# Kernel tuning notes

Hardware: AMD Instinct MI355X
Metric: run time of the kernel (lower is better)

Reference implementation:

```python
import jax, jax.numpy as jnp
from jax import lax
import numpy as np

B, T, DIN, DMID, DOUT = 8, 512, 512, 512, 128
KER = (0.15, 0.7, 0.15)  # 3-tap Gaussian blur, midnum fixed at 0.7 (deterministic stand-in for random.uniform(0.55,0.9))


def setup_inputs() -> dict:
    key = jax.random.key(0)
    ks = jax.random.split(key, 14)
    def lin(k, fi, fo):
        s = (6.0 / (fi + fo)) ** 0.5  # xavier-uniform
        return jax.random.uniform(k, (fi, fo), jnp.float32, -s, s)
    def convw(k, co, ci, kh, kw):
        s = (6.0 / (ci * kh * kw + co * kh * kw)) ** 0.5
        return jax.random.uniform(k, (co, ci, kh, kw), jnp.float32, -s, s)
    return {
        "seq": jax.random.normal(ks[0], (B, T, DIN), jnp.float32),
        "len_seq": jax.random.randint(ks[1], (B,), 256, T + 1, jnp.int32),
        "W1": lin(ks[2], DIN, DMID), "b1": jnp.zeros((DMID,), jnp.float32),
        "W2": lin(ks[3], DMID, DMID), "b2": jnp.zeros((DMID,), jnp.float32),
        "W3": lin(ks[4], DMID, DOUT), "b3": jnp.zeros((DOUT,), jnp.float32),
        "c1w": convw(ks[5], 30, 2, 5, 5), "c1b": jnp.zeros((30,), jnp.float32),
        "c2w": convw(ks[6], 30, 30, 5, 5), "c2b": jnp.zeros((30,), jnp.float32),
        "c3w": convw(ks[7], 1, 30, 3, 3), "c3b": jnp.zeros((1,), jnp.float32),
    }


def _mlp(x, W1, b1, W2, b2, W3, b3):
    # SequenceInception: linear-relu-linear-relu-linear, then L2 normalize with nan/inf -> 0
    h = jax.nn.relu(x @ W1 + b1)
    h = jax.nn.relu(h @ W2 + b2)
    o = h @ W3 + b3
    n = jnp.linalg.norm(o, axis=-1, keepdims=True)
    return jnp.nan_to_num(o / n, nan=0.0, posinf=0.0, neginf=0.0)


def _conv(x, w, b, pad):
    y = lax.conv_general_dilated(x, w, (1, 1), ((pad, pad), (pad, pad)),
                                 dimension_numbers=("NCHW", "OIHW", "NCHW"))
    return y + b[None, :, None, None]


def _blur(seq, len_seq):
    # BlurGenerationPair (Tc>4, 3-tap kernel, stride 1 branch), fully batched.
    k0, k1, k2 = KER
    blur = k0 * seq[:, :-2] + k1 * seq[:, 1:-1] + k2 * seq[:, 2:]  # [B, T-2, D]
    blur = jnp.pad(blur, ((0, 0), (0, 2), (0, 0)))
    t = jnp.arange(T)
    out_len = len_seq - 2
    out_mask = (t[None, :] < out_len[:, None]).astype(seq.dtype)      # [B, T]
    avged_seq = blur * out_mask[:, :, None]
    R = jnp.where(t[None] < len_seq[:, None], (t + 1.0) / len_seq[:, None].astype(jnp.float32), 0.0)
    avged_R = jnp.where(t[None] < out_len[:, None], (t + 1.0) / out_len[:, None].astype(jnp.float32), 0.0)
    # SeqtoBlur[b, i+o, i] = ker[o] for column i < out_len[b]
    base = k0 * jnp.eye(T) + k1 * jnp.eye(T, k=-1) + k2 * jnp.eye(T, k=-2)  # [T(row), T(col)]
    SeqtoBlur = base[None, :, :] * out_mask[:, None, :]
    sg = lax.stop_gradient
    return sg(SeqtoBlur), sg(avged_seq), sg(R), sg(avged_R), out_len


def reference(seq, len_seq, W1, b1, W2, b2, W3, b3, c1w, c1b, c2w, c2b, c3w, c3b):
    SeqtoBlur, avged_seq, R, avged_R, avged_len = _blur(seq, len_seq)
    emb_q = _mlp(seq, W1, b1, W2, b2, W3, b3)        # [B, T, DOUT]
    emb_k = _mlp(avged_seq, W1, b1, W2, b2, W3, b3)  # [B, T, DOUT]
    # OPA, batched over B (original asserts batch==1 and loops; same math per sample)
    sq = jnp.sum(emb_q * emb_q, -1)
    sk = jnp.sum(emb_k * emb_k, -1)
    g = jnp.einsum("bqd,bkd->bqk", emb_q, emb_k)
    D = jnp.sqrt(jnp.clip(sq[:, :, None] + sk[:, None, :] - 2.0 * g, 1e-12))  # cdist p=2
    P = jnp.abs(R[:, :, None] - avged_R[:, None, :])                           # 1-D cdist
    A = jnp.stack([D, P], axis=1)                    # [B, 2, T, T]
    A = jax.nn.relu(_conv(A, c1w, c1b, 2))
    A = jax.nn.relu(_conv(A, c2w, c2b, 2))
    A = _conv(A, c3w, c3b, 1)[:, 0] + D              # [B, T, T]
    S = jax.nn.softmax(-A, axis=2)
    At = S / jnp.sum(jnp.abs(S), axis=(1, 2), keepdims=True)  # L1 normalize over T*T
    dis = jnp.sum(D * At, axis=(1, 2))               # [B]
    return S, dis, SeqtoBlur, avged_len
```

## Files before the change

kernel.cpp:

```cpp
#include <hip/hip_runtime.h>
#include <hip/hip_bf16.h>

static constexpr size_t CHW = (size_t)512*512*32;

static constexpr size_t S_OFF    = 0;
static constexpr size_t DIS_OFF  = (size_t)8*512*512;
static constexpr size_t S2B_OFF  = DIS_OFF + 8;
static constexpr size_t ALEN_OFF = S2B_OFF + (size_t)8*512*512;

typedef __attribute__((ext_vector_type(8))) short bf16x8;
typedef __attribute__((ext_vector_type(4))) float f32x4;
typedef __attribute__((ext_vector_type(2))) float f32x2;
typedef __attribute__((ext_vector_type(4))) int   i32x4;

__device__ __forceinline__ unsigned short rne_bf16(float x) {
  unsigned u = __builtin_bit_cast(unsigned, x);
  return (unsigned short)((u + 0x7FFFu + ((u >> 16) & 1u)) >> 16);
}
__device__ __forceinline__ unsigned pack_bf16x2(float lo, float hi) {
  return (unsigned)rne_bf16(lo) | ((unsigned)rne_bf16(hi) << 16);
}
__device__ __forceinline__ float bf2f(short s) {
  return __builtin_bit_cast(float, ((unsigned)(unsigned short)s) << 16);
}
__device__ __forceinline__ int chlog(int p) { return (p & 1) ? 16 + (p >> 1) : (p >> 1); }

__global__ __launch_bounds__(128) void megaprep(
    const float* __restrict__ seq, const int* __restrict__ len,
    const float* __restrict__ W1, const float* __restrict__ W2, const float* __restrict__ W3,
    const float* __restrict__ c1w, const float* __restrict__ c2w, const float* __restrict__ c3w,
    unsigned short* __restrict__ QKb,
    unsigned short* __restrict__ W1T, unsigned short* __restrict__ W2T,
    unsigned short* __restrict__ W3T,
    unsigned short* __restrict__ WB1m, unsigned char* __restrict__ WB2f,
    float* __restrict__ WT3, float* __restrict__ zpage,
    float* __restrict__ R, float* __restrict__ AR, float* __restrict__ alenOut,
    float* __restrict__ s2b) {
  int bid = blockIdx.x, tid = threadIdx.x;
  if (bid < 8192) {
    int t = bid & 511, b = (bid >> 9) & 7, mode = bid >> 12;
    size_t base = ((size_t)b*512 + t)*512 + tid*4;
    float v[4] = {0.f, 0.f, 0.f, 0.f};
    if (mode == 0) {
      float4 a = *(const float4*)&seq[base];
      v[0]=a.x; v[1]=a.y; v[2]=a.z; v[3]=a.w;
    } else {
      int OL = len[b] - 2;
      if (t < OL) {
        float4 a = *(const float4*)&seq[base];
        float4 c = *(const float4*)&seq[base + 512];
        float4 d = *(const float4*)&seq[base + 1024];
        v[0] = 0.15f*a.x + 0.7f*c.x + 0.15f*d.x;
        v[1] = 0.15f*a.y + 0.7f*c.y + 0.15f*d.y;
        v[2] = 0.15f*a.z + 0.7f*c.z + 0.15f*d.z;
        v[3] = 0.15f*a.w + 0.7f*c.w + 0.15f*d.w;
      }
    }
    ushort4 h;
    h.x = rne_bf16(v[0]); h.y = rne_bf16(v[1]);
    h.z = rne_bf16(v[2]); h.w = rne_bf16(v[3]);
    *(ushort4*)&QKb[((size_t)(mode*4096 + b*512 + t))*512 + tid*4] = h;
    return;
  }
  if (bid < 12288) {
    int r = bid - 8192;
    int i = r & 511, b = r >> 9;
    int OL = len[b] - 2;
    int j0 = tid*4;
    float vals[4];
#pragma unroll
    for (int e = 0; e < 4; ++e) {
      int j = j0 + e;
      float x = 0.f;
      if (j < OL) {
        if (j == i)        x = 0.15f;
        else if (j == i-1) x = 0.7f;
        else if (j == i-2) x = 0.15f;
      }
      vals[e] = x;
    }
    *(float4*)&s2b[((size_t)b*512 + i)*512 + j0] =
        make_float4(vals[0],vals[1],vals[2],vals[3]);
    return;
  }
  if (bid < 12320) {
    int r = bid - 12288;
    int b = r >> 2, t = (r & 3)*128 + tid;
    int L = len[b], OL = L - 2;
    R[b*512+t]  = (t < L)  ? (t+1.f)/(float)L  : 0.f;
    AR[b*512+t] = (t < OL) ? (t+1.f)/(float)OL : 0.f;
    if (t == 0) alenOut[b] = (float)OL;
    return;
  }
  if (bid < 13472) {
    int n = bid - 12320;
    const float* W; unsigned short* WT; int col, N;
    if (n < 512)       { W = W1; WT = W1T; col = n;        N = 512; }
    else if (n < 1024) { W = W2; WT = W2T; col = n - 512;  N = 512; }
    else               { W = W3; WT = W3T; col = n - 1024; N = 128; }
    for (int k = tid; k < 512; k += 128)
      WT[(size_t)col*512 + k] = rne_bf16(W[(size_t)k*N + col]);
    return;
  }
  if (tid < 64) zpage[tid] = 0.f;
  for (int i = tid; i < 7168; i += 128) {
    int ts = i >> 8, r = i & 255, oc = r >> 3, ch = r & 7;
    float v = 0.f;
    if (ts < 25 && oc < 30 && ch < 2) v = c1w[oc*50 + ch*25 + ts];
    WB1m[i] = rne_bf16(v);
  }
  for (int i = tid; i < 12800; i += 128) {
    int tap = i >> 9, r = i & 511, oc = r >> 4, jj = r & 15;
    float v0 = (oc < 30 && jj < 30)      ? c2w[(size_t)(oc*30 + jj)*25 + tap]      : 0.f;
    float v1 = (oc < 30 && 16 + jj < 30) ? c2w[(size_t)(oc*30 + 16 + jj)*25 + tap] : 0.f;
    int pk = __builtin_amdgcn_cvt_pk_fp8_f32(v0, v1, 0, false);
    ((unsigned short*)WB2f)[(tap*32 + oc)*16 + jj] = (unsigned short)pk;
  }
  for (int i = tid; i < 288; i += 128) {
    int tap = i >> 5, icp = i & 31;
    int icl = chlog(icp);
    WT3[i] = (icl < 30) ? c3w[icl*9 + tap] : 0.f;
  }
}

template<int OUTMODE>
__global__ __launch_bounds__(256) void gemm_bf(
    const unsigned short* __restrict__ A, const unsigned short* __restrict__ B,
    const float* __restrict__ bias, float* __restrict__ Cf,
    unsigned short* __restrict__ Cb, int M, int N, int K) {
  __shared__ short sA[128*40], sB[64*40];
  int tid = threadIdx.x, l = tid & 63, w = tid >> 6;
  int wm = w >> 1, wn = w & 1;
  int rowBase = blockIdx.y * 128, colBase = blockIdx.x * 64;
  int lr = l & 15, lc = l >> 4;
  f32x4 acc[4][2] = {};
  for (int k0 = 0; k0 < K; k0 += 32) {
    int idx = tid;
#pragma unroll
    for (int it = 0; it < 2; ++it, idx += 256) {
      int row = idx >> 2, c = (idx & 3) * 8;
      *(bf16x8*)&sA[row*40 + c] = *(const bf16x8*)&A[(size_t)(rowBase + row)*K + k0 + c];
    }
    {
      int row = tid >> 2, c = (tid & 3) * 8;
      if (row < 64)
        *(bf16x8*)&sB[row*40 + c] = *(const bf16x8*)&B[(size_t)(colBase + row)*K + k0 + c];
    }
    __syncthreads();
    bf16x8 a[4], b[2];
#pragma unroll
    for (int m = 0; m < 4; ++m)
      a[m] = *(const bf16x8*)&sA[(wm*64 + m*16 + lr)*40 + lc*8];
#pragma unroll
    for (int n = 0; n < 2; ++n)
      b[n] = *(const bf16x8*)&sB[(wn*32 + n*16 + lr)*40 + lc*8];
#pragma unroll
    for (int m = 0; m < 4; ++m)
#pragma unroll
      for (int n = 0; n < 2; ++n)
        acc[m][n] = __builtin_amdgcn_mfma_f32_16x16x32_bf16(a[m], b[n], acc[m][n], 0, 0, 0);
    __syncthreads();
  }
#pragma unroll
  for (int m = 0; m < 4; ++m) {
    int row = rowBase + wm*64 + m*16 + lc*4;
#pragma unroll
    for (int n = 0; n < 2; ++n) {
      int col = colBase + wn*32 + n*16 + lr;
      float bv = bias[col];
#pragma unroll
      for (int j = 0; j < 4; ++j) {
        float v = acc[m][n][j] + bv;
        size_t o = (size_t)(row + j) * N + col;
        if (OUTMODE == 1) Cb[o] = rne_bf16(fmaxf(v, 0.f));
        else              Cf[o] = v;
      }
    }
  }
}

__global__ __launch_bounds__(64) void norm_kernel(const float* __restrict__ EMB,
    unsigned short* __restrict__ Eb, float* __restrict__ sqn) {
  int row = blockIdx.x, tid = threadIdx.x;
  size_t base = (size_t)row * 128;
  float v0 = EMB[base + tid], v1 = EMB[base + tid + 64];
  float ss = v0*v0 + v1*v1;
#pragma unroll
  for (int off = 32; off; off >>= 1) ss += __shfl_xor(ss, off);
  float n = sqrtf(ss);
  float inv = (n > 0.f) ? 1.f/n : 0.f;
  Eb[base + tid]      = rne_bf16(v0 * inv);
  Eb[base + tid + 64] = rne_bf16(v1 * inv);
  if (tid == 0) sqn[row] = ss * inv * inv;
}

__global__ __launch_bounds__(256) void dmat_mfma(const unsigned short* __restrict__ Eb,
    const float* __restrict__ sqn, float* __restrict__ Dm) {
  __shared__ short sQ[64*40], sK[64*40];
  int tid = threadIdx.x, l = tid & 63, w = tid >> 6;
  int wm = w >> 1, wn = w & 1;
  int kBase = blockIdx.x * 64, qBase = blockIdx.y * 64, b = blockIdx.z;
  const unsigned short* Q  = Eb + (size_t)b*512*128;
  const unsigned short* Kp = Eb + (size_t)(4096 + b*512)*128;
  int lr = l & 15, lc = l >> 4;
  f32x4 acc[2][2] = {};
  for (int k0 = 0; k0 < 128; k0 += 32) {
    int row = tid >> 2, c = (tid & 3) * 8;
    *(bf16x8*)&sQ[row*40 + c] = *(const bf16x8*)&Q[(size_t)(qBase + row)*128 + k0 + c];
    *(bf16x8*)&sK[row*40 + c] = *(const bf16x8*)&Kp[(size_t)(kBase + row)*128 + k0 + c];
    __syncthreads();
    bf16x8 q[2], k[2];
#pragma unroll
    for (int m = 0; m < 2; ++m) q[m] = *(const bf16x8*)&sQ[(wm*32 + m*16 + lr)*40 + lc*8];
#pragma unroll
    for (int n = 0; n < 2; ++n) k[n] = *(const bf16x8*)&sK[(wn*32 + n*16 + lr)*40 + lc*8];
#pragma unroll
    for (int m = 0; m < 2; ++m)
#pragma unroll
      for (int n = 0; n < 2; ++n)
        acc[m][n] = __builtin_amdgcn_mfma_f32_16x16x32_bf16(q[m], k[n], acc[m][n], 0, 0, 0);
    __syncthreads();
  }
#pragma unroll
  for (int m = 0; m < 2; ++m) {
#pragma unroll
    for (int n = 0; n < 2; ++n) {
      int k = kBase + wn*32 + n*16 + lr;
      float skv = sqn[4096 + b*512 + k];
#pragma unroll
      for (int j = 0; j < 4; ++j) {
        int q = qBase + wm*32 + m*16 + lc*4 + j;
        float sqv = sqn[b*512 + q];
        float d2 = fmaxf(sqv + skv - 2.f*acc[m][n][j], 1e-12f);
        Dm[((size_t)b*512 + q)*512 + k] = sqrtf(d2);
      }
    }
  }
}

__global__ __launch_bounds__(256) void conv1_mfma(const float* __restrict__ Dm,
    const float* __restrict__ R, const float* __restrict__ AR,
    unsigned char* __restrict__ cbout, const unsigned short* __restrict__ WB1m,
    const float* __restrict__ bias, int b0) {
  __shared__ short tile[36*20*8];
  int tid = threadIdx.x, l = tid & 63, w = tid >> 6;
  int x0 = blockIdx.x * 16, y0 = blockIdx.y * 32, slot = blockIdx.z;
  int b = b0 + slot;
  for (int i = tid; i < 720; i += 256) {
    int r = i / 20, c = i - r*20;
    int gy = y0 - 2 + r, gx = x0 - 2 + c;
    float dv = 0.f, pv = 0.f;
    if ((unsigned)gy < 512u && (unsigned)gx < 512u) {
      dv = Dm[((size_t)b*512 + gy)*512 + gx];
      pv = fabsf(R[b*512 + gy] - AR[b*512 + gx]);
    }
    bf16x8 v = {};
    v[0] = (short)rne_bf16(dv);
    v[1] = (short)rne_bf16(pv);
    *(bf16x8*)&tile[i*8] = v;
  }
  __syncthreads();
  int lr = l & 15, lc = l >> 4;
  f32x4 acc[8][2] = {};
  int wy = w * 8;
  bf16x8 pb0 = *(const bf16x8*)&WB1m[(size_t)lc*256 + lr*8];
  bf16x8 pb1 = *(const bf16x8*)&WB1m[(size_t)lc*256 + (16 + lr)*8];
  __builtin_amdgcn_s_setprio(1);
#pragma unroll
  for (int m = 0; m < 7; ++m) {
    int t = m*4 + lc;
    int ky = t / 5, kx = t - ky*5;
    bool valid = (t < 25);
    bf16x8 b0 = pb0, b1 = pb1;
    if (m < 6) {
      int tn = (m+1)*4 + lc;
      pb0 = *(const bf16x8*)&WB1m[(size_t)tn*256 + lr*8];
      pb1 = *(const bf16x8*)&WB1m[(size_t)tn*256 + (16 + lr)*8];
    }
#pragma unroll
    for (int g = 0; g < 8; ++g) {
      bf16x8 a = {};
      if (valid) a = *(const bf16x8*)&tile[((wy + g + ky)*20 + lr + kx)*8];
      acc[g][0] = __builtin_amdgcn_mfma_f32_16x16x32_bf16(a, b0, acc[g][0], 0, 0, 0);
      acc[g][1] = __builtin_amdgcn_mfma_f32_16x16x32_bf16(a, b1, acc[g][1], 0, 0, 0);
    }
  }
  __builtin_amdgcn_s_setprio(0);
  unsigned char* outp = cbout + (size_t)slot * CHW;
  float bv0 = bias[lr];
  float bv1 = (16 + lr < 30) ? bias[16 + lr] : 0.f;
#pragma unroll
  for (int g = 0; g < 8; ++g) {
    int y = y0 + wy + g;
#pragma unroll
    for (int j = 0; j < 4; ++j) {
      int px = x0 + lc*4 + j;
      size_t ob = ((size_t)y*512 + px)*32;
      int pk = __builtin_amdgcn_cvt_pk_fp8_f32(
          fmaxf(acc[g][0][j] + bv0, 0.f), fmaxf(acc[g][1][j] + bv1, 0.f), 0, false);
      *(unsigned short*)&outp[ob + 2*lr] = (unsigned short)pk;
    }
  }
}

__global__ __launch_bounds__(256, 4) void conv2_mfma(const unsigned char* __restrict__ cbin,
    unsigned char* __restrict__ cbout, const unsigned char* __restrict__ WB2f,
    const float* __restrict__ bias, const float* __restrict__ zpage) {
  __shared__ char tile[36*20*32];
  int tid = threadIdx.x, l = tid & 63, w = tid >> 6;
  int x0 = blockIdx.x * 16, y0 = blockIdx.y * 32, slot = blockIdx.z;
  const unsigned char* in = cbin + (size_t)slot * CHW;
  for (int idx = tid; idx < 1440; idx += 256) {
    int cs = idx & 1, px = idx >> 1;
    int r = px / 20, cc = px - r*20;
    int c16 = cs ^ ((cc >> 1) & 1);
    int gy = y0 - 2 + r, gx = x0 - 2 + cc;
    const void* src = ((unsigned)gy < 512u && (unsigned)gx < 512u)
        ? (const void*)&in[((size_t)gy*512 + gx)*32 + c16*16]
        : (const void*)zpage;
    __builtin_amdgcn_global_load_lds(
        (const __attribute__((address_space(1))) void*)src,
        (__attribute__((address_space(3))) void*)&tile[(size_t)idx*16], 16, 0, 0);
  }
  __syncthreads();
  int lr = l & 15, lc = l >> 4;
  f32x4 acc[8][2] = {};
  int wy = w * 8;
  long long pb0[2], pb1[2];
  {
    pb0[0] = *(const long long*)&WB2f[(size_t)(0*32 + lr)*32 + lc*8];
    pb1[0] = *(const long long*)&WB2f[(size_t)(0*32 + 16 + lr)*32 + lc*8];
    pb0[1] = *(const long long*)&WB2f[(size_t)(5*32 + lr)*32 + lc*8];
    pb1[1] = *(const long long*)&WB2f[(size_t)(5*32 + 16 + lr)*32 + lc*8];
  }
  __builtin_amdgcn_s_setprio(1);
#pragma unroll
  for (int kx = 0; kx < 5; ++kx) {
    int x = lr + kx;
    int s = (((lc >> 1) ^ ((x >> 1) & 1)) << 1) | (lc & 1);
    long long a[12];
#pragma unroll
    for (int r = 0; r < 12; ++r)
      a[r] = *(const long long*)&tile[((wy + r)*20 + x)*32 + s*8];
#pragma unroll
    for (int ky = 0; ky < 5; ++ky) {
      int i = kx*5 + ky;
      int sq = i & 1;
      long long b0 = pb0[sq], b1 = pb1[sq];
      int in2 = i + 2;
      if (in2 < 25) {
        int nkx = in2 / 5, nky = in2 - nkx*5;
        int ntap = nky*5 + nkx;
        pb0[sq] = *(const long long*)&WB2f[(size_t)(ntap*32 + lr)*32 + lc*8];
        pb1[sq] = *(const long long*)&WB2f[(size_t)(ntap*32 + 16 + lr)*32 + lc*8];
      }
#pragma unroll
      for (int g = 0; g < 8; ++g) {
        acc[g][0] = __builtin_amdgcn_mfma_f32_16x16x32_fp8_fp8(a[g+ky], b0, acc[g][0], 0, 0, 0);
        acc[g][1] = __builtin_amdgcn_mfma_f32_16x16x32_fp8_fp8(a[g+ky], b1, acc[g][1], 0, 0, 0);
      }
    }
  }
  __builtin_amdgcn_s_setprio(0);
  unsigned char* outp = cbout + (size_t)slot * CHW;
  float bv0 = (lr < 30) ? bias[lr] : 0.f;
  float bv1 = 0.f;
  if (16 + lr < 30) bv1 = bias[16 + lr];
#pragma unroll
  for (int g = 0; g < 8; ++g) {
    int y = y0 + wy + g;
#pragma unroll
    for (int j = 0; j < 4; ++j) {
      int px = x0 + lc*4 + j;
      size_t ob = ((size_t)y*512 + px)*32;
      int pk = __builtin_amdgcn_cvt_pk_fp8_f32(
          fmaxf(acc[g][0][j] + bv0, 0.f), fmaxf(acc[g][1][j] + bv1, 0.f), 0, false);
      *(unsigned short*)&outp[ob + 2*lr] = (unsigned short)pk;
    }
  }
}

__global__ __launch_bounds__(256) void conv3_nhwc(const unsigned char* __restrict__ cbin,
    const float* __restrict__ Dm, const float* __restrict__ WT3,
    const float* __restrict__ b3c, float* __restrict__ A3, int b0) {
  int slot = blockIdx.z, b = b0 + slot;
  int tid = threadIdx.x, tx = tid & 15, ty = tid >> 4;
  int x0 = blockIdx.x * 16, y0 = blockIdx.y * 16;
  __shared__ char tile[18*18*40];
  const unsigned char* in = cbin + (size_t)slot * CHW;
  for (int idx = tid; idx < 648; idx += 256) {
    int c = idx & 1, px = idx >> 1;
    int r = px / 18, cc = px - r*18;
    int gy = y0 - 1 + r, gx = x0 - 1 + cc;
    i32x4 v = {};
    if ((unsigned)gy < 512u && (unsigned)gx < 512u)
      v = *(const i32x4*)&in[((size_t)gy*512 + gx)*32 + c*16];
    *(i32x4*)&tile[px*40 + c*16] = v;
  }
  __syncthreads();
  float acc = 0.f;
#pragma unroll
  for (int ky = 0; ky < 3; ++ky) {
#pragma unroll
    for (int kx = 0; kx < 3; ++kx) {
      const float* wp = &WT3[(ky*3 + kx)*32];
      int base = ((ty+ky)*18 + tx+kx)*40;
      i32x4 v0 = *(const i32x4*)&tile[base];
      i32x4 v1 = *(const i32x4*)&tile[base + 16];
#pragma unroll
      for (int q = 0; q < 4; ++q) {
        f32x2 f0 = __builtin_amdgcn_cvt_pk_f32_fp8(v0[q], false);
        f32x2 f1 = __builtin_amdgcn_cvt_pk_f32_fp8(v0[q], true);
        acc = fmaf(f0[0], wp[q*4+0], acc);
        acc = fmaf(f0[1], wp[q*4+1], acc);
        acc = fmaf(f1[0], wp[q*4+2], acc);
        acc = fmaf(f1[1], wp[q*4+3], acc);
        f32x2 g0 = __builtin_amdgcn_cvt_pk_f32_fp8(v1[q], false);
        f32x2 g1 = __builtin_amdgcn_cvt_pk_f32_fp8(v1[q], true);
        acc = fmaf(g0[0], wp[16 + q*4+0], acc);
        acc = fmaf(g0[1], wp[16 + q*4+1], acc);
        acc = fmaf(g1[0], wp[16 + q*4+2], acc);
        acc = fmaf(g1[1], wp[16 + q*4+3], acc);
      }
    }
  }
  size_t o = ((size_t)b*512 + y0 + ty)*512 + x0 + tx;
  A3[o] = acc + b3c[0] + Dm[o];
}

__global__ __launch_bounds__(256) void softmax_kernel(const float* __restrict__ A3,
    const float* __restrict__ Dm, float* __restrict__ S,
    float* __restrict__ rowDS, float* __restrict__ rowSS) {
  __shared__ float sred[4];
  __shared__ float sred2[4], sred3[4];
  int q = blockIdx.x, b = blockIdx.y, tid = threadIdx.x;
  size_t base = ((size_t)b*512 + q)*512;
  float x0 = -A3[base + tid], x1 = -A3[base + tid + 256];
  float m = fmaxf(x0, x1);
#pragma unroll
  for (int off = 32; off; off >>= 1) m = fmaxf(m, __shfl_xor(m, off));
  if ((tid & 63) == 0) sred[tid >> 6] = m;
  __syncthreads();
  m = fmaxf(fmaxf(sred[0], sred[1]), fmaxf(sred[2], sred[3]));
  __syncthreads();
  float p0 = expf(x0 - m), p1 = expf(x1 - m);
  float s = p0 + p1;
#pragma unroll
  for (int off = 32; off; off >>= 1) s += __shfl_xor(s, off);
  if ((tid & 63) == 0) sred[tid >> 6] = s;
  __syncthreads();
  s = sred[0] + sred[1] + sred[2] + sred[3];
  float inv = 1.f / s;
  float s0 = p0 * inv, s1 = p1 * inv;
  S[base + tid] = s0;
  S[base + tid + 256] = s1;
  float ds = s0*Dm[base + tid] + s1*Dm[base + tid + 256];
  float ssum = s0 + s1;
#pragma unroll
  for (int off = 32; off; off >>= 1) { ds += __shfl_xor(ds, off); ssum += __shfl_xor(ssum, off); }
  if ((tid & 63) == 0) { sred2[tid>>6] = ds; sred3[tid>>6] = ssum; }
  __syncthreads();
  if (tid == 0) {
    rowDS[b*512+q] = sred2[0]+sred2[1]+sred2[2]+sred2[3];
    rowSS[b*512+q] = sred3[0]+sred3[1]+sred3[2]+sred3[3];
  }
}

__global__ __launch_bounds__(512) void dis_kernel(const float* __restrict__ rowDS,
    const float* __restrict__ rowSS, float* __restrict__ disOut) {
  __shared__ float sd[8], se[8];
  int b = blockIdx.x, tid = threadIdx.x;
  float ds = rowDS[b*512 + tid];
  float ss = rowSS[b*512 + tid];
#pragma unroll
  for (int off = 32; off; off >>= 1) { ds += __shfl_xor(ds, off); ss += __shfl_xor(ss, off); }
  if ((tid & 63) == 0) { sd[tid>>6] = ds; se[tid>>6] = ss; }
  __syncthreads();
  if (tid == 0) {
    float a = 0.f, c = 0.f;
    for (int i = 0; i < 8; ++i) { a += sd[i]; c += se[i]; }
    disOut[b] = a / c;
  }
}

extern "C" void kernel_launch(void* const* d_in, const int* in_sizes, int n_in,
                              void* d_out, int out_size, void* d_ws, size_t ws_size,
                              hipStream_t stream) {
  const float* seq = (const float*)d_in[0];
  const int*   len = (const int*)d_in[1];
  const float* W1  = (const float*)d_in[2];  const float* b1 = (const float*)d_in[3];
  const float* W2  = (const float*)d_in[4];  const float* b2 = (const float*)d_in[5];
  const float* W3  = (const float*)d_in[6];  const float* b3 = (const float*)d_in[7];
  const float* c1w = (const float*)d_in[8];  const float* c1b = (const float*)d_in[9];
  const float* c2w = (const float*)d_in[10]; const float* c2b = (const float*)d_in[11];
  const float* c3w = (const float*)d_in[12]; const float* c3b = (const float*)d_in[13];
  float* out = (float*)d_out;
  char*  ws  = (char*)d_ws;

  size_t off = 0;
  auto alloc = [&](size_t bytes) { size_t o = off; off = (off + bytes + 255) & ~(size_t)255; return o; };
  const size_t MK2 = (size_t)8192*512*2;
  unsigned short* QKb = (unsigned short*)(ws + alloc(MK2));
  unsigned short* H1  = (unsigned short*)(ws + alloc(MK2));
  unsigned short* H2  = (unsigned short*)(ws + alloc(MK2));
  float* EMB = (float*)(ws + alloc((size_t)8192*128*4));
  unsigned short* EMBb = (unsigned short*)(ws + alloc((size_t)8192*128*2));
  float* SQN = (float*)(ws + alloc(8192*4));
  float* Rb  = (float*)(ws + alloc(4096*4));
  float* ARb = (float*)(ws + alloc(4096*4));
  float* Db  = (float*)(ws + alloc((size_t)8*512*512*4));
  float* A3  = (float*)(ws + alloc((size_t)8*512*512*4));
  float* RDS = (float*)(ws + alloc(4096*4));
  float* RSS = (float*)(ws + alloc(4096*4));
  unsigned short* W1T = (unsigned short*)(ws + alloc((size_t)512*512*2));
  unsigned short* W2T = (unsigned short*)(ws + alloc((size_t)512*512*2));
  unsigned short* W3T = (unsigned short*)(ws + alloc((size_t)128*512*2));
  unsigned short* WB1m = (unsigned short*)(ws + alloc(7168*2));
  unsigned char* WB2f = (unsigned char*)(ws + alloc(25600));
  float* WT3 = (float*)(ws + alloc(288*4));
  float* ZPG = (float*)(ws + alloc(256));
  size_t fixed = off;

  int nb = 1;
  const size_t CBB = CHW;
  if      (fixed + 8*2*CBB <= ws_size) nb = 8;
  else if (fixed + 4*2*CBB <= ws_size) nb = 4;
  else if (fixed + 2*2*CBB <= ws_size) nb = 2;
  unsigned char* CB1 = (unsigned char*)(ws + alloc((size_t)nb*CBB));
  unsigned char* CB2 = (unsigned char*)(ws + alloc((size_t)nb*CBB));

  megaprep<<<13473, 128, 0, stream>>>(seq, len, W1, W2, W3, c1w, c2w, c3w,
      QKb, W1T, W2T, W3T, WB1m, WB2f, WT3, ZPG, Rb, ARb, out + ALEN_OFF, out + S2B_OFF);

  gemm_bf<1><<<dim3(8, 64), 256, 0, stream>>>(QKb, W1T, b1, nullptr, H1, 8192, 512, 512);
  gemm_bf<1><<<dim3(8, 64), 256, 0, stream>>>(H1,  W2T, b2, nullptr, H2, 8192, 512, 512);
  gemm_bf<0><<<dim3(2, 64), 256, 0, stream>>>(H2,  W3T, b3, EMB, nullptr, 8192, 128, 512);
  norm_kernel<<<8192, 64, 0, stream>>>(EMB, EMBb, SQN);
  dmat_mfma<<<dim3(8,8,8), 256, 0, stream>>>(EMBb, SQN, Db);

  for (int bb = 0; bb < 8; bb += nb) {
    conv1_mfma<<<dim3(32,16,nb), 256, 0, stream>>>(Db, Rb, ARb, CB1, WB1m, c1b, bb);
    conv2_mfma<<<dim3(32,16,nb), 256, 0, stream>>>(CB1, CB2, WB2f, c2b, ZPG);
    conv3_nhwc<<<dim3(32,32,nb), 256, 0, stream>>>(CB2, Db, WT3, c3b, A3, bb);
  }

  softmax_kernel<<<dim3(512,8), 256, 0, stream>>>(A3, Db, out + S_OFF, RDS, RSS);
  dis_kernel<<<8, 512, 0, stream>>>(RDS, RSS, out + DIS_OFF);
}
```

Baseline: 250.9 us.

## Store D and A3 in bf16 and double-buffer conv2 tiles per block

The distance matrix D and the conv3 output A3 are now stored as bf16 instead of fp32, which halves the intermediate traffic read by conv1, conv3 and softmax. conv2 now processes two 32-row tiles per block. It issues the async global-to-LDS load for the second tile before computing the first, so load latency overlaps with MFMA work. This doubles LDS per block and lowers the occupancy hint from 4 to 3 blocks. The bf16 storage also reduces precision of D used in the softmax and dis outputs.

Measured after the change: 270.4 us. 1.08x slower.

```diff
diff --git a/kernel.cpp b/kernel.cpp
--- a/kernel.cpp
+++ b/kernel.cpp
@@ -17,10 +17,10 @@
   unsigned u = __builtin_bit_cast(unsigned, x);
   return (unsigned short)((u + 0x7FFFu + ((u >> 16) & 1u)) >> 16);
 }
-__device__ __forceinline__ unsigned pack_bf16x2(float lo, float hi) {
-  return (unsigned)rne_bf16(lo) | ((unsigned)rne_bf16(hi) << 16);
-}
-__device__ __forceinline__ float bf2f(short s) {
+__device__ __forceinline__ float bf2f(unsigned short s) {
+  return __builtin_bit_cast(float, ((unsigned)s) << 16);
+}
+__device__ __forceinline__ float bf2fs(short s) {
   return __builtin_bit_cast(float, ((unsigned)(unsigned short)s) << 16);
 }
 __device__ __forceinline__ int chlog(int p) { return (p & 1) ? 16 + (p >> 1) : (p >> 1); }
@@ -195,7 +195,7 @@
 }
 
 __global__ __launch_bounds__(256) void dmat_mfma(const unsigned short* __restrict__ Eb,
-    const float* __restrict__ sqn, float* __restrict__ Dm) {
+    const float* __restrict__ sqn, unsigned short* __restrict__ Dm) {
   __shared__ short sQ[64*40], sK[64*40];
   int tid = threadIdx.x, l = tid & 63, w = tid >> 6;
   int wm = w >> 1, wn = w & 1;
@@ -232,13 +232,13 @@
         int q = qBase + wm*32 + m*16 + lc*4 + j;
         float sqv = sqn[b*512 + q];
         float d2 = fmaxf(sqv + skv - 2.f*acc[m][n][j], 1e-12f);
-        Dm[((size_t)b*512 + q)*512 + k] = sqrtf(d2);
+        Dm[((size_t)b*512 + q)*512 + k] = rne_bf16(sqrtf(d2));
       }
     }
   }
 }
 
-__global__ __launch_bounds__(256) void conv1_mfma(const float* __restrict__ Dm,
+__global__ __launch_bounds__(256) void conv1_mfma(const unsigned short* __restrict__ Dm,
     const float* __restrict__ R, const float* __restrict__ AR,
     unsigned char* __restrict__ cbout, const unsigned short* __restrict__ WB1m,
     const float* __restrict__ bias, int b0) {
@@ -251,7 +251,7 @@
     int gy = y0 - 2 + r, gx = x0 - 2 + c;
     float dv = 0.f, pv = 0.f;
     if ((unsigned)gy < 512u && (unsigned)gx < 512u) {
-      dv = Dm[((size_t)b*512 + gy)*512 + gx];
+      dv = bf2f(Dm[((size_t)b*512 + gy)*512 + gx]);
       pv = fabsf(R[b*512 + gy] - AR[b*512 + gx]);
     }
     bf16x8 v = {};
@@ -303,86 +303,98 @@
   }
 }
 
-__global__ __launch_bounds__(256, 4) void conv2_mfma(const unsigned char* __restrict__ cbin,
+#define CONV2_STAGE(TILE, Y0)                                                   \
+  for (int idx = tid; idx < 1440; idx += 256) {                                 \
+    int cs = idx & 1, px = idx >> 1;                                            \
+    int r = px / 20, cc = px - r*20;                                            \
+    int c16 = cs ^ ((cc >> 1) & 1);                                             \
+    int gy = (Y0) - 2 + r, gx = x0 - 2 + cc;                                    \
+    const void* src = ((unsigned)gy < 512u && (unsigned)gx < 512u)              \
+        ? (const void*)&in[((size_t)gy*512 + gx)*32 + c16*16]                   \
+        : (const void*)zpage;                                                   \
+    __builtin_amdgcn_global_load_lds(                                           \
+        (const __attribute__((address_space(1))) void*)src,                     \
+        (__attribute__((address_space(3))) void*)&TILE[(size_t)idx*16], 16, 0, 0); \
+  }
+
+#define CONV2_COMPUTE(TILE, Y0)                                                 \
+  {                                                                             \
+    f32x4 acc[8][2] = {};                                                       \
+    int wy = w * 8;                                                             \
+    long long pb0[2], pb1[2];                                                   \
+    pb0[0] = *(const long long*)&WB2f[(size_t)(0*32 + lr)*32 + lc*8];           \
+    pb1[0] = *(const long long*)&WB2f[(size_t)(0*32 + 16 + lr)*32 + lc*8];      \
+    pb0[1] = *(const long long*)&WB2f[(size_t)(5*32 + lr)*32 + lc*8];           \
+    pb1[1] = *(const long long*)&WB2f[(size_t)(5*32 + 16 + lr)*32 + lc*8];      \
+    __builtin_amdgcn_s_setprio(1);                                              \
+    _Pragma("unroll")                                                           \
+    for (int kx = 0; kx < 5; ++kx) {                                            \
+      int x = lr + kx;                                                          \
+      int s = (((lc >> 1) ^ ((x >> 1) & 1)) << 1) | (lc & 1);                   \
+      long long a[12];                                                          \
+      _Pragma("unroll")                                                         \
+      for (int r = 0; r < 12; ++r)                                              \
+        a[r] = *(const long long*)&TILE[((wy + r)*20 + x)*32 + s*8];            \
+      _Pragma("unroll")                                                         \
+      for (int ky = 0; ky < 5; ++ky) {                                          \
+        int i = kx*5 + ky;                                                      \
+        int sq = i & 1;                                                         \
+        long long b0 = pb0[sq], b1 = pb1[sq];                                   \
+        int in2 = i + 2;                                                        \
+        if (in2 < 25) {                                                         \
+          int nkx = in2 / 5, nky = in2 - nkx*5;                                 \
+          int ntap = nky*5 + nkx;                                               \
+          pb0[sq] = *(const long long*)&WB2f[(size_t)(ntap*32 + lr)*32 + lc*8]; \
+          pb1[sq] = *(const long long*)&WB2f[(size_t)(ntap*32 + 16 + lr)*32 + lc*8]; \
+        }                                                                       \
+        _Pragma("unroll")                                                       \
+        for (int g = 0; g < 8; ++g) {                                           \
+          acc[g][0] = __builtin_amdgcn_mfma_f32_16x16x32_fp8_fp8(a[g+ky], b0, acc[g][0], 0, 0, 0); \
+          acc[g][1] = __builtin_amdgcn_mfma_f32_16x16x32_fp8_fp8(a[g+ky], b1, acc[g][1], 0, 0, 0); \
+        }                                                                       \
+      }                                                                         \
+    }                                                                           \
+    __builtin_amdgcn_s_setprio(0);                                              \
+    _Pragma("unroll")                                                           \
+    for (int g = 0; g < 8; ++g) {                                               \
+      int y = (Y0) + wy + g;                                                    \
+      _Pragma("unroll")                                                         \
+      for (int j = 0; j < 4; ++j) {                                             \
+        int px = x0 + lc*4 + j;                                                 \
+        size_t ob = ((size_t)y*512 + px)*32;                                    \
+        int pk = __builtin_amdgcn_cvt_pk_fp8_f32(                               \
+            fmaxf(acc[g][0][j] + bv0, 0.f), fmaxf(acc[g][1][j] + bv1, 0.f), 0, false); \
+        *(unsigned short*)&outp[ob + 2*lr] = (unsigned short)pk;                \
+      }                                                                         \
+    }                                                                           \
+  }
+
+__global__ __launch_bounds__(256, 3) void conv2_mfma(const unsigned char* __restrict__ cbin,
     unsigned char* __restrict__ cbout, const unsigned char* __restrict__ WB2f,
     const float* __restrict__ bias, const float* __restrict__ zpage) {
-  __shared__ char tile[36*20*32];
+  __shared__ char tileA[36*20*32];
+  __shared__ char tileB[36*20*32];
   int tid = threadIdx.x, l = tid & 63, w = tid >> 6;
-  int x0 = blockIdx.x * 16, y0 = blockIdx.y * 32, slot = blockIdx.z;
+  int x0 = blockIdx.x * 16, slot = blockIdx.z;
+  int y0a = blockIdx.y * 64, y0b = y0a + 32;
   const unsigned char* in = cbin + (size_t)slot * CHW;
-  for (int idx = tid; idx < 1440; idx += 256) {
-    int cs = idx & 1, px = idx >> 1;
-    int r = px / 20, cc = px - r*20;
-    int c16 = cs ^ ((cc >> 1) & 1);
-    int gy = y0 - 2 + r, gx = x0 - 2 + cc;
-    const void* src = ((unsigned)gy < 512u && (unsigned)gx < 512u)
-        ? (const void*)&in[((size_t)gy*512 + gx)*32 + c16*16]
-        : (const void*)zpage;
-    __builtin_amdgcn_global_load_lds(
-        (const __attribute__((address_space(1))) void*)src,
-        (__attribute__((address_space(3))) void*)&tile[(size_t)idx*16], 16, 0, 0);
-  }
-  __syncthreads();
+  unsigned char* outp = cbout + (size_t)slot * CHW;
   int lr = l & 15, lc = l >> 4;
-  f32x4 acc[8][2] = {};
-  int wy = w * 8;
-  long long pb0[2], pb1[2];
-  {
-    pb0[0] = *(const long long*)&WB2f[(size_t)(0*32 + lr)*32 + lc*8];
-    pb1[0] = *(const long long*)&WB2f[(size_t)(0*32 + 16 + lr)*32 + lc*8];
-    pb0[1] = *(const long long*)&WB2f[(size_t)(5*32 + lr)*32 + lc*8];
-    pb1[1] = *(const long long*)&WB2f[(size_t)(5*32 + 16 + lr)*32 + lc*8];
-  }
-  __builtin_amdgcn_s_setprio(1);
-#pragma unroll
-  for (int kx = 0; kx < 5; ++kx) {
-    int x = lr + kx;
-    int s = (((lc >> 1) ^ ((x >> 1) & 1)) << 1) | (lc & 1);
-    long long a[12];
-#pragma unroll
-    for (int r = 0; r < 12; ++r)
-      a[r] = *(const long long*)&tile[((wy + r)*20 + x)*32 + s*8];
-#pragma unroll
-    for (int ky = 0; ky < 5; ++ky) {
-      int i = kx*5 + ky;
-      int sq = i & 1;
-      long long b0 = pb0[sq], b1 = pb1[sq];
-      int in2 = i + 2;
-      if (in2 < 25) {
-        int nkx = in2 / 5, nky = in2 - nkx*5;
-        int ntap = nky*5 + nkx;
-        pb0[sq] = *(const long long*)&WB2f[(size_t)(ntap*32 + lr)*32 + lc*8];
-        pb1[sq] = *(const long long*)&WB2f[(size_t)(ntap*32 + 16 + lr)*32 + lc*8];
-      }
-#pragma unroll
-      for (int g = 0; g < 8; ++g) {
-        acc[g][0] = __builtin_amdgcn_mfma_f32_16x16x32_fp8_fp8(a[g+ky], b0, acc[g][0], 0, 0, 0);
-        acc[g][1] = __builtin_amdgcn_mfma_f32_16x16x32_fp8_fp8(a[g+ky], b1, acc[g][1], 0, 0, 0);
-      }
-    }
-  }
-  __builtin_amdgcn_s_setprio(0);
-  unsigned char* outp = cbout + (size_t)slot * CHW;
   float bv0 = (lr < 30) ? bias[lr] : 0.f;
   float bv1 = 0.f;
   if (16 + lr < 30) bv1 = bias[16 + lr];
-#pragma unroll
-  for (int g = 0; g < 8; ++g) {
-    int y = y0 + wy + g;
-#pragma unroll
-    for (int j = 0; j < 4; ++j) {
-      int px = x0 + lc*4 + j;
-      size_t ob = ((size_t)y*512 + px)*32;
-      int pk = __builtin_amdgcn_cvt_pk_fp8_f32(
-          fmaxf(acc[g][0][j] + bv0, 0.f), fmaxf(acc[g][1][j] + bv1, 0.f), 0, false);
-      *(unsigned short*)&outp[ob + 2*lr] = (unsigned short)pk;
-    }
-  }
+
+  CONV2_STAGE(tileA, y0a)
+  __syncthreads();
+  CONV2_STAGE(tileB, y0b)
+  CONV2_COMPUTE(tileA, y0a)
+  __syncthreads();
+  CONV2_COMPUTE(tileB, y0b)
 }
 
 __global__ __launch_bounds__(256) void conv3_nhwc(const unsigned char* __restrict__ cbin,
-    const float* __restrict__ Dm, const float* __restrict__ WT3,
-    const float* __restrict__ b3c, float* __restrict__ A3, int b0) {
+    const unsigned short* __restrict__ Dm, const float* __restrict__ WT3,
+    const float* __restrict__ b3c, unsigned short* __restrict__ A3, int b0) {
   int slot = blockIdx.z, b = b0 + slot;
   int tid = threadIdx.x, tx = tid & 15, ty = tid >> 4;
   int x0 = blockIdx.x * 16, y0 = blockIdx.y * 16;
@@ -425,17 +437,17 @@
     }
   }
   size_t o = ((size_t)b*512 + y0 + ty)*512 + x0 + tx;
-  A3[o] = acc + b3c[0] + Dm[o];
-}
-
-__global__ __launch_bounds__(256) void softmax_kernel(const float* __restrict__ A3,
-    const float* __restrict__ Dm, float* __restrict__ S,
+  A3[o] = rne_bf16(acc + b3c[0] + bf2f(Dm[o]));
+}
+
+__global__ __launch_bounds__(256) void softmax_kernel(const unsigned short* __restrict__ A3,
+    const unsigned short* __restrict__ Dm, float* __restrict__ S,
     float* __restrict__ rowDS, float* __restrict__ rowSS) {
   __shared__ float sred[4];
   __shared__ float sred2[4], sred3[4];
   int q = blockIdx.x, b = blockIdx.y, tid = threadIdx.x;
   size_t base = ((size_t)b*512 + q)*512;
-  float x0 = -A3[base + tid], x1 = -A3[base + tid + 256];
+  float x0 = -bf2f(A3[base + tid]), x1 = -bf2f(A3[base + tid + 256]);
   float m = fmaxf(x0, x1);
 #pragma unroll
   for (int off = 32; off; off >>= 1) m = fmaxf(m, __shfl_xor(m, off));
@@ -454,7 +466,7 @@
   float s0 = p0 * inv, s1 = p1 * inv;
   S[base + tid] = s0;
   S[base + tid + 256] = s1;
-  float ds = s0*Dm[base + tid] + s1*Dm[base + tid + 256];
+  float ds = s0*bf2f(Dm[base + tid]) + s1*bf2f(Dm[base + tid + 256]);
   float ssum = s0 + s1;
 #pragma unroll
   for (int off = 32; off; off >>= 1) { ds += __shfl_xor(ds, off); ssum += __shfl_xor(ssum, off); }
@@ -508,8 +520,8 @@
   float* SQN = (float*)(ws + alloc(8192*4));
   float* Rb  = (float*)(ws + alloc(4096*4));
   float* ARb = (float*)(ws + alloc(4096*4));
-  float* Db  = (float*)(ws + alloc((size_t)8*512*512*4));
-  float* A3  = (float*)(ws + alloc((size_t)8*512*512*4));
+  unsigned short* Db = (unsigned short*)(ws + alloc((size_t)8*512*512*2));
+  unsigned short* A3 = (unsigned short*)(ws + alloc((size_t)8*512*512*2));
   float* RDS = (float*)(ws + alloc(4096*4));
   float* RSS = (float*)(ws + alloc(4096*4));
   unsigned short* W1T = (unsigned short*)(ws + alloc((size_t)512*512*2));
@@ -540,7 +552,7 @@
 
   for (int bb = 0; bb < 8; bb += nb) {
     conv1_mfma<<<dim3(32,16,nb), 256, 0, stream>>>(Db, Rb, ARb, CB1, WB1m, c1b, bb);
-    conv2_mfma<<<dim3(32,16,nb), 256, 0, stream>>>(CB1, CB2, WB2f, c2b, ZPG);
+    conv2_mfma<<<dim3(32,8,nb), 256, 0, stream>>>(CB1, CB2, WB2f, c2b, ZPG);
     conv3_nhwc<<<dim3(32,32,nb), 256, 0, stream>>>(CB2, Db, WT3, c3b, A3, bb);
   }
 
```
